# Performance work log

Hardware: AMD Instinct MI355X
Metric: run time of the kernel (lower is better)

Reference implementation:

```python
import jax, jax.numpy as jnp
import numpy as np

MASS = 2.0
B, DIN, H, DOUT = 32768, 4, 128, 5


def setup_inputs():
    key = jax.random.key(0)
    ks = jax.random.split(key, 5)
    def w(k, shp, fan):
        return jax.random.normal(k, shp, jnp.float32) * (1.0 / np.sqrt(fan))
    return {
        "x": jax.random.normal(ks[0], (B, DIN), jnp.float32),
        "W0": w(ks[1], (DIN, H), DIN), "b0": jnp.zeros((H,), jnp.float32),
        "W1": w(ks[2], (H, H), H), "b1": jnp.zeros((H,), jnp.float32),
        "W2": w(ks[3], (H, H), H), "b2": jnp.zeros((H,), jnp.float32),
        "W3": w(ks[4], (H, DOUT), H), "b3": jnp.zeros((DOUT,), jnp.float32),
    }


def _mlp_outs(xs, params):
    # xs: [4] = (t, x, y, z)
    h = xs
    for W, b in params[:-1]:
        h = jnp.tanh(h @ W + b)
    W, b = params[-1]
    o = h @ W + b  # [5]
    return o[:1], o[1:4], o[4:5]  # n [1], v [3], Fi [1]


def _per_sample(xs, params, m):
    outs = lambda z: _mlp_outs(z, params)

    def firsts(z):
        n, v, Fi = outs(z)
        ro = m * n
        return n, n * v, Fi, ro, ro * v  # n, j, Fi, ro, rov

    # all first-order jacobians in one jacfwd pass (4 tangents)
    n_jac, j_jac, Fi_jac, ro_jac, rov_jac = jax.jacfwd(firsts)(xs)

    def pair(z):
        o = outs(z)
        return o[0], o[2]  # n, Fi

    n_hess, Fi_hess = jax.jacfwd(jax.jacfwd(pair))(xs)  # [1,4,4] each

    n, v, Fi = outs(xs)
    n_t = n_jac[..., 0]                                  # [1]
    n_grd = n_jac[..., 1:4]                              # [1,3]
    j = n * v                                            # [3]
    j_div = jnp.sum(j_jac[..., 1:4], axis=-1)            # [3]
    Fi_grd = Fi_jac[..., 1:4]                            # [1,3]
    Fi_lap = jnp.sum(Fi_hess[..., 1:4], axis=-1)         # [1,4]
    # faithful to source: v_jac = batch_jacobian(n, input)  (verbatim bug)
    v_jac = n_jac                                        # [1,4]
    v_t = v_jac[..., 0]                                  # [1]
    v_adv = jnp.sum(v[None, :] * v_jac[..., 1:4], axis=-2)  # [3]
    v_div_jac = jnp.sum(n_hess[:, 1:4, :], axis=1)       # [1,4]
    v_div_grd = v_div_jac[..., 1:4]                      # [1,3]
    v_lap = jnp.trace(n_hess[..., 1:4], axis1=-2, axis2=-1)  # [1]
    ro = m * n                                           # [1]
    ro_t = ro_jac[..., 0]                                # [1]
    ro_grd = ro_jac[..., 1:4]                            # [1,3]
    rov_div = jnp.sum(rov_jac[..., 1:4], axis=-1)        # [3]
    return (n, n_t, n_grd, j, j_div, Fi, Fi_grd, Fi_lap,
            v, v_t, v_adv, v_lap, v_div_grd, ro, ro_t, ro_grd, rov_div)


def reference(x, W0, b0, W1, b1, W2, b2, W3, b3):
    params = [(W0, b0), (W1, b1), (W2, b2), (W3, b3)]
    return jax.vmap(lambda xs: _per_sample(xs, params, MASS))(x)
```

## Files before the change

kernel.cpp:

```cpp
#include <hip/hip_runtime.h>
#include <hip/hip_bf16.h>


namespace {

constexpr int HID = 128;

using bf16x8 = __attribute__((ext_vector_type(8))) short;
using f32x4  = __attribute__((ext_vector_type(4))) float;
typedef unsigned       __attribute__((may_alias)) u32a;
typedef unsigned short __attribute__((may_alias)) u16a;

#define LDS_FENCE() asm volatile("" ::: "memory")

struct OSpec {
    int base, mul, off;
    int a0, a1, a2, m;
    int b0, b1, b2, m2;
    float s1, s2;
};

__constant__ OSpec g_ospec[38] = {
    {0,1,0,   0,80,80,81, 80,80,80,81, 1.f,0.f},
    {1,1,0,   5,80,80,81, 80,80,80,81, 1.f,0.f},
    {2,3,0,  10,80,80,81, 80,80,80,81, 1.f,0.f},
    {2,3,1,  15,80,80,81, 80,80,80,81, 1.f,0.f},
    {2,3,2,  20,80,80,81, 80,80,80,81, 1.f,0.f},
    {5,3,0,   1,80,80, 0, 80,80,80,81, 1.f,0.f},
    {5,3,1,   2,80,80, 0, 80,80,80,81, 1.f,0.f},
    {5,3,2,   3,80,80, 0, 80,80,80,81, 1.f,0.f},
    {8,3,0,  10,15,20, 1, 11,16,21, 0, 1.f,1.f},
    {8,3,1,  10,15,20, 2, 12,17,22, 0, 1.f,1.f},
    {8,3,2,  10,15,20, 3, 13,18,23, 0, 1.f,1.f},
    {11,1,0,  4,80,80,81, 80,80,80,81, 1.f,0.f},
    {12,3,0, 14,80,80,81, 80,80,80,81, 1.f,0.f},
    {12,3,1, 19,80,80,81, 80,80,80,81, 1.f,0.f},
    {12,3,2, 24,80,80,81, 80,80,80,81, 1.f,0.f},
    {15,4,0, 34,39,44,81, 80,80,80,81, 1.f,0.f},
    {15,4,1, 49,54,59,81, 80,80,80,81, 1.f,0.f},
    {15,4,2, 54,64,69,81, 80,80,80,81, 1.f,0.f},
    {15,4,3, 59,69,74,81, 80,80,80,81, 1.f,0.f},
    {19,3,0,  1,80,80,81, 80,80,80,81, 1.f,0.f},
    {19,3,1,  2,80,80,81, 80,80,80,81, 1.f,0.f},
    {19,3,2,  3,80,80,81, 80,80,80,81, 1.f,0.f},
    {22,1,0,  5,80,80,81, 80,80,80,81, 1.f,0.f},
    {23,3,0,  1,80,80,10, 80,80,80,81, 1.f,0.f},
    {23,3,1,  2,80,80,15, 80,80,80,81, 1.f,0.f},
    {23,3,2,  3,80,80,20, 80,80,80,81, 1.f,0.f},
    {26,1,0, 30,50,65,81, 80,80,80,81, 1.f,0.f},
    {27,3,0, 45,50,55,81, 80,80,80,81, 1.f,0.f},
    {27,3,1, 50,60,65,81, 80,80,80,81, 1.f,0.f},
    {27,3,2, 55,65,70,81, 80,80,80,81, 1.f,0.f},
    {30,1,0,  0,80,80,81, 80,80,80,81, 2.f,0.f},
    {31,1,0,  5,80,80,81, 80,80,80,81, 2.f,0.f},
    {32,3,0, 10,80,80,81, 80,80,80,81, 2.f,0.f},
    {32,3,1, 15,80,80,81, 80,80,80,81, 2.f,0.f},
    {32,3,2, 20,80,80,81, 80,80,80,81, 2.f,0.f},
    {35,3,0, 10,15,20, 1, 11,16,21, 0, 2.f,2.f},
    {35,3,1, 10,15,20, 2, 12,17,22, 0, 2.f,2.f},
    {35,3,2, 10,15,20, 3, 13,18,23, 0, 2.f,2.f},
};

__device__ __forceinline__ unsigned short f2bf(float f) {
    union { float f; unsigned u; } v; v.f = f;
    unsigned r = v.u + 0x7FFFu + ((v.u >> 16) & 1u);
    return (unsigned short)(r >> 16);
}
__device__ __forceinline__ unsigned pk_bf16(float lo, float hi) {
    __bf16 l = (__bf16)lo;
    __bf16 h = (__bf16)hi;
    unsigned short ul, uh;
    __builtin_memcpy(&ul, &l, 2);
    __builtin_memcpy(&uh, &h, 2);
    return (unsigned)ul | ((unsigned)uh << 16);
}
__device__ __forceinline__ float tanh_fast(float z) {
    float e = __builtin_amdgcn_exp2f(z * 2.8853900817779268f);
    return 1.0f - 2.0f * __builtin_amdgcn_rcpf(e + 1.0f);
}
__device__ __forceinline__ int swz(int row, int byte_in_row) {
    return (row * 256 + byte_in_row) ^ ((row & 7) << 4);
}

__global__ void pack_w_kernel(const float* __restrict__ W1,
                              const float* __restrict__ W2,
                              const float* __restrict__ W3,
                              unsigned short* __restrict__ wsB) {
    int t = blockIdx.x * 256 + threadIdx.x;
    if (t < 32768) {
        int reg  = t & 7;
        int lane = (t >> 3) & 63;
        int nt   = (t >> 9) & 7;
        int kt   = (t >> 12) & 3;
        int layer = (t >> 14) & 1;
        int k = kt * 32 + (lane >> 4) * 8 + reg;
        int n = nt * 16 + (lane & 15);
        const float* W = layer ? W2 : W1;
        wsB[t] = f2bf(W[k * HID + n]);
    } else if (t < 34816) {
        int tt = t - 32768;
        int reg  = tt & 7;
        int lane = (tt >> 3) & 63;
        int kt   = (tt >> 9) & 3;
        int k = kt * 32 + (lane >> 4) * 8 + reg;
        int n = lane & 15;
        wsB[t] = (n < 5) ? f2bf(W3[k * 5 + n]) : (unsigned short)0;
    }
}

__global__ __launch_bounds__(256, 4) void mlp_pde_kernel(
    const float* __restrict__ x,
    const float* __restrict__ W0, const float* __restrict__ b0,
    const float* __restrict__ b1, const float* __restrict__ b2,
    const float* __restrict__ b3,
    const unsigned short* __restrict__ wsB,
    float* __restrict__ out, int nb)
{
    constexpr int PD[10] = {0,0,0,0,1,1,1,2,2,3};
    constexpr int PE[10] = {0,1,2,3,1,2,3,2,3,3};

    __shared__ float lds[4][2048];
    const int wave = threadIdx.x >> 6;
    const int lane = threadIdx.x & 63;
    float* wbase = lds[wave];
    char* abufA = (char*)wbase;
    char* abufB = (char*)wbase + 4096;
    float* combA = wbase;
    float* combB = wbase + 82;
    int bA = blockIdx.x * 8 + wave * 2;
    int bB = bA + 1;
    if (bA >= nb) bA = nb - 1;
    if (bB >= nb) bB = nb - 1;

    {
        const int j0 = lane * 2;
        float w0d[4][2];
        #pragma unroll
        for (int d = 0; d < 4; ++d) {
            float2 w = *reinterpret_cast<const float2*>(W0 + d * HID + j0);
            w0d[d][0] = w.x; w0d[d][1] = w.y;
        }
        const float2 bb0 = *reinterpret_cast<const float2*>(b0 + j0);
        const float4 xvA = *reinterpret_cast<const float4*>(x + 4 * bA);
        const float4 xvB = *reinterpret_cast<const float4*>(x + 4 * bB);
        #pragma unroll
        for (int s = 0; s < 2; ++s) {
            const float4 xv = s ? xvB : xvA;
            char* abuf = s ? abufB : abufA;
            float val[15][2];
            #pragma unroll
            for (int jj = 0; jj < 2; ++jj) {
                float z = ((jj == 0) ? bb0.x : bb0.y)
                        + xv.x * w0d[0][jj] + xv.y * w0d[1][jj]
                        + xv.z * w0d[2][jj] + xv.w * w0d[3][jj];
                float h = tanh_fast(z);
                float sd = 1.f - h * h;
                val[0][jj] = h;
                #pragma unroll
                for (int d = 0; d < 4; ++d) val[1 + d][jj] = sd * w0d[d][jj];
                #pragma unroll
                for (int p = 0; p < 10; ++p)
                    val[5 + p][jj] = -2.f * h * sd * w0d[PD[p]][jj] * w0d[PE[p]][jj];
            }
            #pragma unroll
            for (int v = 0; v < 15; ++v)
                *reinterpret_cast<u32a*>(abuf + swz(v, j0 * 2)) = pk_bf16(val[v][0], val[v][1]);
            *reinterpret_cast<u32a*>(abuf + swz(15, j0 * 2)) = 0u;
        }
    }
    LDS_FENCE();

    const int jloc = lane & 15;
    const int rgrp = lane >> 4;

    auto recomb = [&](const f32x4& acc, char* abuf, float bnt, int nt) {
        float z0 = __shfl(acc[0], jloc, 64);
        float u0 = __shfl(acc[1], jloc, 64);
        float u1 = __shfl(acc[2], jloc, 64);
        float u2 = __shfl(acc[3], jloc, 64);
        float u3 = __shfl(acc[0], jloc + 16, 64);
        float h = tanh_fast(z0 + bnt);
        float s = 1.f - h * h;
        float c = -2.f * h * s;
        float nv[4];
        if (rgrp == 0) {
            nv[0] = h;           nv[1] = s * u0;
            nv[2] = s * u1;      nv[3] = s * u2;
        } else if (rgrp == 1) {
            nv[0] = s * u3;
            nv[1] = fmaf(c * u0, u0, s * acc[1]);
            nv[2] = fmaf(c * u0, u1, s * acc[2]);
            nv[3] = fmaf(c * u0, u2, s * acc[3]);
        } else if (rgrp == 2) {
            nv[0] = fmaf(c * u0, u3, s * acc[0]);
            nv[1] = fmaf(c * u1, u1, s * acc[1]);
            nv[2] = fmaf(c * u1, u2, s * acc[2]);
            nv[3] = fmaf(c * u1, u3, s * acc[3]);
        } else {
            nv[0] = fmaf(c * u2, u2, s * acc[0]);
            nv[1] = fmaf(c * u2, u3, s * acc[1]);
            nv[2] = fmaf(c * u3, u3, s * acc[2]);
            nv[3] = 0.f;
        }
        unsigned pk01 = pk_bf16(nv[0], nv[1]);
        unsigned pk23 = pk_bf16(nv[2], nv[3]);
        const int bcol = (nt * 16 + jloc) * 2;
        *reinterpret_cast<u16a*>(abuf + swz(rgrp * 4 + 0, bcol)) = (unsigned short)pk01;
        *reinterpret_cast<u16a*>(abuf + swz(rgrp * 4 + 1, bcol)) = (unsigned short)(pk01 >> 16);
        *reinterpret_cast<u16a*>(abuf + swz(rgrp * 4 + 2, bcol)) = (unsigned short)pk23;
        *reinterpret_cast<u16a*>(abuf + swz(rgrp * 4 + 3, bcol)) = (unsigned short)(pk23 >> 16);
    };

    #pragma unroll 1
    for (int layer = 0; layer < 2; ++layer) {
        bf16x8 a0[4], a1[4];
        #pragma unroll
        for (int kt = 0; kt < 4; ++kt) {
            a0[kt] = *reinterpret_cast<const bf16x8*>(abufA + swz(jloc, kt * 64 + rgrp * 16));
            a1[kt] = *reinterpret_cast<const bf16x8*>(abufB + swz(jloc, kt * 64 + rgrp * 16));
        }
        LDS_FENCE();
        const float* bias = layer ? b2 : b1;
        float bv[8];
        #pragma unroll
        for (int nt = 0; nt < 8; ++nt) bv[nt] = bias[nt * 16 + jloc];

        #pragma unroll
        for (int nt = 0; nt < 8; ++nt) {
            f32x4 acc0 = {0.f, 0.f, 0.f, 0.f};
            f32x4 acc1 = {0.f, 0.f, 0.f, 0.f};
            #pragma unroll
            for (int kt = 0; kt < 4; ++kt) {
                bf16x8 bfrag = *reinterpret_cast<const bf16x8*>(
                    wsB + ((size_t)((layer * 4 + kt) * 8 + nt) * 512 + lane * 8));
                acc0 = __builtin_amdgcn_mfma_f32_16x16x32_bf16(a0[kt], bfrag, acc0, 0, 0, 0);
                acc1 = __builtin_amdgcn_mfma_f32_16x16x32_bf16(a1[kt], bfrag, acc1, 0, 0, 0);
            }
            recomb(acc0, abufA, bv[nt], nt);
            recomb(acc1, abufB, bv[nt], nt);
        }
        LDS_FENCE();
    }

    bf16x8 t0[4], t1[4];
    #pragma unroll
    for (int kt = 0; kt < 4; ++kt) {
        t0[kt] = *reinterpret_cast<const bf16x8*>(abufA + swz(jloc, kt * 64 + rgrp * 16));
        t1[kt] = *reinterpret_cast<const bf16x8*>(abufB + swz(jloc, kt * 64 + rgrp * 16));
    }
    LDS_FENCE();

    f32x4 f0 = {0.f, 0.f, 0.f, 0.f};
    f32x4 f1 = {0.f, 0.f, 0.f, 0.f};
    #pragma unroll
    for (int kt = 0; kt < 4; ++kt) {
        bf16x8 w3f = *reinterpret_cast<const bf16x8*>(
            wsB + 32768 + (size_t)(kt * 64 + lane) * 8);
        f0 = __builtin_amdgcn_mfma_f32_16x16x32_bf16(t0[kt], w3f, f0, 0, 0, 0);
        f1 = __builtin_amdgcn_mfma_f32_16x16x32_bf16(t1[kt], w3f, f1, 0, 0, 0);
    }

    if (jloc < 5) {
        #pragma unroll
        for (int q = 0; q < 4; ++q) {
            int row = rgrp * 4 + q;
            float tA = f0[q];
            float tB = f1[q];
            if (row == 0) { float bb = b3[jloc]; tA += bb; tB += bb; }
            combA[row * 5 + jloc] = tA;
            combB[row * 5 + jloc] = tB;
        }
    }
    if (lane == 63) { combA[80] = 0.f; combA[81] = 1.f; combB[80] = 0.f; combB[81] = 1.f; }
    LDS_FENCE();

    if (lane < 38) {
        OSpec sp = g_ospec[lane];
        float a1v = (combA[sp.a0] + combA[sp.a1] + combA[sp.a2]) * combA[sp.m] * sp.s1;
        float a2v = (combA[sp.b0] + combA[sp.b1] + combA[sp.b2]) * combA[sp.m2] * sp.s2;
        out[sp.base * nb + bA * sp.mul + sp.off] = a1v + a2v;
        float c1v = (combB[sp.a0] + combB[sp.a1] + combB[sp.a2]) * combB[sp.m] * sp.s1;
        float c2v = (combB[sp.b0] + combB[sp.b1] + combB[sp.b2]) * combB[sp.m2] * sp.s2;
        out[sp.base * nb + bB * sp.mul + sp.off] = c1v + c2v;
    }
}

}

extern "C" void kernel_launch(void* const* d_in, const int* in_sizes, int n_in,
                              void* d_out, int out_size, void* d_ws, size_t ws_size,
                              hipStream_t stream) {
    const float* x  = (const float*)d_in[0];
    const float* W0 = (const float*)d_in[1];
    const float* b0 = (const float*)d_in[2];
    const float* W1 = (const float*)d_in[3];
    const float* b1 = (const float*)d_in[4];
    const float* W2 = (const float*)d_in[5];
    const float* b2 = (const float*)d_in[6];
    const float* W3 = (const float*)d_in[7];
    const float* b3 = (const float*)d_in[8];
    float* out = (float*)d_out;
    unsigned short* wsB = (unsigned short*)d_ws;

    const int nb = in_sizes[0] / 4;
    pack_w_kernel<<<136, 256, 0, stream>>>(W1, W2, W3, wsB);
    const int blocks = (nb + 7) / 8;
    mlp_pde_kernel<<<blocks, 256, 0, stream>>>(x, W0, b0, b1, b2, b3, wsB, out, nb);
}
```

Measured before the change: 82.83 us.

## Switch hidden-layer MFMAs to 32x32x16 tiles covering both samples per wave

```diff
diff --git a/kernel.cpp b/kernel.cpp
--- a/kernel.cpp
+++ b/kernel.cpp
@@ -7,7 +7,7 @@
 constexpr int HID = 128;
 
 using bf16x8 = __attribute__((ext_vector_type(8))) short;
-using f32x4  = __attribute__((ext_vector_type(4))) float;
+using f32x16 = __attribute__((ext_vector_type(16))) float;
 typedef unsigned       __attribute__((may_alias)) u32a;
 typedef unsigned short __attribute__((may_alias)) u16a;
 
@@ -23,42 +23,42 @@
 __constant__ OSpec g_ospec[38] = {
     {0,1,0,   0,80,80,81, 80,80,80,81, 1.f,0.f},
     {1,1,0,   5,80,80,81, 80,80,80,81, 1.f,0.f},
-    {2,3,0,  10,80,80,81, 80,80,80,81, 1.f,0.f},
-    {2,3,1,  15,80,80,81, 80,80,80,81, 1.f,0.f},
-    {2,3,2,  20,80,80,81, 80,80,80,81, 1.f,0.f},
+    {2,3,0,  25,80,80,81, 80,80,80,81, 1.f,0.f},
+    {2,3,1,  10,80,80,81, 80,80,80,81, 1.f,0.f},
+    {2,3,2,  30,80,80,81, 80,80,80,81, 1.f,0.f},
     {5,3,0,   1,80,80, 0, 80,80,80,81, 1.f,0.f},
     {5,3,1,   2,80,80, 0, 80,80,80,81, 1.f,0.f},
     {5,3,2,   3,80,80, 0, 80,80,80,81, 1.f,0.f},
-    {8,3,0,  10,15,20, 1, 11,16,21, 0, 1.f,1.f},
-    {8,3,1,  10,15,20, 2, 12,17,22, 0, 1.f,1.f},
-    {8,3,2,  10,15,20, 3, 13,18,23, 0, 1.f,1.f},
+    {8,3,0,  25,10,30, 1, 26,11,31, 0, 1.f,1.f},
+    {8,3,1,  25,10,30, 2, 27,12,32, 0, 1.f,1.f},
+    {8,3,2,  25,10,30, 3, 28,13,33, 0, 1.f,1.f},
     {11,1,0,  4,80,80,81, 80,80,80,81, 1.f,0.f},
-    {12,3,0, 14,80,80,81, 80,80,80,81, 1.f,0.f},
-    {12,3,1, 19,80,80,81, 80,80,80,81, 1.f,0.f},
-    {12,3,2, 24,80,80,81, 80,80,80,81, 1.f,0.f},
-    {15,4,0, 34,39,44,81, 80,80,80,81, 1.f,0.f},
-    {15,4,1, 49,54,59,81, 80,80,80,81, 1.f,0.f},
-    {15,4,2, 54,64,69,81, 80,80,80,81, 1.f,0.f},
-    {15,4,3, 59,69,74,81, 80,80,80,81, 1.f,0.f},
+    {12,3,0, 29,80,80,81, 80,80,80,81, 1.f,0.f},
+    {12,3,1, 14,80,80,81, 80,80,80,81, 1.f,0.f},
+    {12,3,2, 34,80,80,81, 80,80,80,81, 1.f,0.f},
+    {15,4,0, 39,44,64,81, 80,80,80,81, 1.f,0.f},
+    {15,4,1, 49,69,54,81, 80,80,80,81, 1.f,0.f},
+    {15,4,2, 69,74,59,81, 80,80,80,81, 1.f,0.f},
+    {15,4,3, 54,59,79,81, 80,80,80,81, 1.f,0.f},
     {19,3,0,  1,80,80,81, 80,80,80,81, 1.f,0.f},
     {19,3,1,  2,80,80,81, 80,80,80,81, 1.f,0.f},
     {19,3,2,  3,80,80,81, 80,80,80,81, 1.f,0.f},
     {22,1,0,  5,80,80,81, 80,80,80,81, 1.f,0.f},
-    {23,3,0,  1,80,80,10, 80,80,80,81, 1.f,0.f},
-    {23,3,1,  2,80,80,15, 80,80,80,81, 1.f,0.f},
-    {23,3,2,  3,80,80,20, 80,80,80,81, 1.f,0.f},
-    {26,1,0, 30,50,65,81, 80,80,80,81, 1.f,0.f},
-    {27,3,0, 45,50,55,81, 80,80,80,81, 1.f,0.f},
-    {27,3,1, 50,60,65,81, 80,80,80,81, 1.f,0.f},
-    {27,3,2, 55,65,70,81, 80,80,80,81, 1.f,0.f},
+    {23,3,0,  1,80,80,25, 80,80,80,81, 1.f,0.f},
+    {23,3,1,  2,80,80,10, 80,80,80,81, 1.f,0.f},
+    {23,3,2,  3,80,80,30, 80,80,80,81, 1.f,0.f},
+    {26,1,0, 35,65,55,81, 80,80,80,81, 1.f,0.f},
+    {27,3,0, 45,65,50,81, 80,80,80,81, 1.f,0.f},
+    {27,3,1, 65,70,55,81, 80,80,80,81, 1.f,0.f},
+    {27,3,2, 50,55,75,81, 80,80,80,81, 1.f,0.f},
     {30,1,0,  0,80,80,81, 80,80,80,81, 2.f,0.f},
     {31,1,0,  5,80,80,81, 80,80,80,81, 2.f,0.f},
-    {32,3,0, 10,80,80,81, 80,80,80,81, 2.f,0.f},
-    {32,3,1, 15,80,80,81, 80,80,80,81, 2.f,0.f},
-    {32,3,2, 20,80,80,81, 80,80,80,81, 2.f,0.f},
-    {35,3,0, 10,15,20, 1, 11,16,21, 0, 2.f,2.f},
-    {35,3,1, 10,15,20, 2, 12,17,22, 0, 2.f,2.f},
-    {35,3,2, 10,15,20, 3, 13,18,23, 0, 2.f,2.f},
+    {32,3,0, 25,80,80,81, 80,80,80,81, 2.f,0.f},
+    {32,3,1, 10,80,80,81, 80,80,80,81, 2.f,0.f},
+    {32,3,2, 30,80,80,81, 80,80,80,81, 2.f,0.f},
+    {35,3,0, 25,10,30, 1, 26,11,31, 0, 2.f,2.f},
+    {35,3,1, 25,10,30, 2, 27,12,32, 0, 2.f,2.f},
+    {35,3,2, 25,10,30, 3, 28,13,33, 0, 2.f,2.f},
 };
 
 __device__ __forceinline__ unsigned short f2bf(float f) {
@@ -74,6 +74,10 @@
     __builtin_memcpy(&uh, &h, 2);
     return (unsigned)ul | ((unsigned)uh << 16);
 }
+__device__ __forceinline__ unsigned short bf1(float x) {
+    __bf16 b = (__bf16)x;
+    unsigned short u; __builtin_memcpy(&u, &b, 2); return u;
+}
 __device__ __forceinline__ float tanh_fast(float z) {
     float e = __builtin_amdgcn_exp2f(z * 2.8853900817779268f);
     return 1.0f - 2.0f * __builtin_amdgcn_rcpf(e + 1.0f);
@@ -88,22 +92,22 @@
                               unsigned short* __restrict__ wsB) {
     int t = blockIdx.x * 256 + threadIdx.x;
     if (t < 32768) {
-        int reg  = t & 7;
-        int lane = (t >> 3) & 63;
-        int nt   = (t >> 9) & 7;
-        int kt   = (t >> 12) & 3;
+        int reg   = t & 7;
+        int lane  = (t >> 3) & 63;
+        int tile  = (t >> 9) & 3;
+        int kt    = (t >> 11) & 7;
         int layer = (t >> 14) & 1;
-        int k = kt * 32 + (lane >> 4) * 8 + reg;
-        int n = nt * 16 + (lane & 15);
+        int k = kt * 16 + ((lane >> 5) & 1) * 8 + reg;
+        int n = tile * 32 + (lane & 31);
         const float* W = layer ? W2 : W1;
         wsB[t] = f2bf(W[k * HID + n]);
-    } else if (t < 34816) {
+    } else if (t < 36864) {
         int tt = t - 32768;
         int reg  = tt & 7;
         int lane = (tt >> 3) & 63;
-        int kt   = (tt >> 9) & 3;
-        int k = kt * 32 + (lane >> 4) * 8 + reg;
-        int n = lane & 15;
+        int kt   = (tt >> 9) & 7;
+        int k = kt * 16 + ((lane >> 5) & 1) * 8 + reg;
+        int n = lane & 31;
         wsB[t] = (n < 5) ? f2bf(W3[k * 5 + n]) : (unsigned short)0;
     }
 }
@@ -118,6 +122,8 @@
 {
     constexpr int PD[10] = {0,0,0,0,1,1,1,2,2,3};
     constexpr int PE[10] = {0,1,2,3,1,2,3,2,3,3};
+    constexpr int ROWMAP[15] = {0,1,5,2,6,3,7,8,12,9,13,10,14,11,15};
+    constexpr int RB[8] = {0,1,2,3,8,9,10,11};
 
     __shared__ float lds[4][2048];
     const int wave = threadIdx.x >> 6;
@@ -164,111 +170,112 @@
             }
             #pragma unroll
             for (int v = 0; v < 15; ++v)
-                *reinterpret_cast<u32a*>(abuf + swz(v, j0 * 2)) = pk_bf16(val[v][0], val[v][1]);
-            *reinterpret_cast<u32a*>(abuf + swz(15, j0 * 2)) = 0u;
+                *reinterpret_cast<u32a*>(abuf + swz(ROWMAP[v], j0 * 2)) =
+                    pk_bf16(val[v][0], val[v][1]);
+            *reinterpret_cast<u32a*>(abuf + swz(4, j0 * 2)) = 0u;
         }
     }
     LDS_FENCE();
 
-    const int jloc = lane & 15;
-    const int rgrp = lane >> 4;
-
-    auto recomb = [&](const f32x4& acc, char* abuf, float bnt, int nt) {
-        float z0 = __shfl(acc[0], jloc, 64);
-        float u0 = __shfl(acc[1], jloc, 64);
-        float u1 = __shfl(acc[2], jloc, 64);
-        float u2 = __shfl(acc[3], jloc, 64);
-        float u3 = __shfl(acc[0], jloc + 16, 64);
-        float h = tanh_fast(z0 + bnt);
-        float s = 1.f - h * h;
-        float c = -2.f * h * s;
-        float nv[4];
-        if (rgrp == 0) {
-            nv[0] = h;           nv[1] = s * u0;
-            nv[2] = s * u1;      nv[3] = s * u2;
-        } else if (rgrp == 1) {
-            nv[0] = s * u3;
-            nv[1] = fmaf(c * u0, u0, s * acc[1]);
-            nv[2] = fmaf(c * u0, u1, s * acc[2]);
-            nv[3] = fmaf(c * u0, u2, s * acc[3]);
-        } else if (rgrp == 2) {
-            nv[0] = fmaf(c * u0, u3, s * acc[0]);
-            nv[1] = fmaf(c * u1, u1, s * acc[1]);
-            nv[2] = fmaf(c * u1, u2, s * acc[2]);
-            nv[3] = fmaf(c * u1, u3, s * acc[3]);
-        } else {
-            nv[0] = fmaf(c * u2, u2, s * acc[0]);
-            nv[1] = fmaf(c * u2, u3, s * acc[1]);
-            nv[2] = fmaf(c * u3, u3, s * acc[2]);
-            nv[3] = 0.f;
-        }
-        unsigned pk01 = pk_bf16(nv[0], nv[1]);
-        unsigned pk23 = pk_bf16(nv[2], nv[3]);
-        const int bcol = (nt * 16 + jloc) * 2;
-        *reinterpret_cast<u16a*>(abuf + swz(rgrp * 4 + 0, bcol)) = (unsigned short)pk01;
-        *reinterpret_cast<u16a*>(abuf + swz(rgrp * 4 + 1, bcol)) = (unsigned short)(pk01 >> 16);
-        *reinterpret_cast<u16a*>(abuf + swz(rgrp * 4 + 2, bcol)) = (unsigned short)pk23;
-        *reinterpret_cast<u16a*>(abuf + swz(rgrp * 4 + 3, bcol)) = (unsigned short)(pk23 >> 16);
-    };
+    const int col  = lane & 31;
+    const int hi   = lane >> 5;
+    const int arow = lane & 15;
+    char* abufM = (char*)wbase + ((lane >> 4) & 1) * 4096;
 
     #pragma unroll 1
     for (int layer = 0; layer < 2; ++layer) {
-        bf16x8 a0[4], a1[4];
-        #pragma unroll
-        for (int kt = 0; kt < 4; ++kt) {
-            a0[kt] = *reinterpret_cast<const bf16x8*>(abufA + swz(jloc, kt * 64 + rgrp * 16));
-            a1[kt] = *reinterpret_cast<const bf16x8*>(abufB + swz(jloc, kt * 64 + rgrp * 16));
+        bf16x8 af[8];
+        #pragma unroll
+        for (int kt = 0; kt < 8; ++kt)
+            af[kt] = *reinterpret_cast<const bf16x8*>(
+                abufM + swz(arow, kt * 32 + hi * 16));
+        LDS_FENCE();
+        const float* bias = layer ? b2 : b1;
+        float bv[4];
+        #pragma unroll
+        for (int t4 = 0; t4 < 4; ++t4) bv[t4] = bias[t4 * 32 + col];
+
+        #pragma unroll
+        for (int t4 = 0; t4 < 4; ++t4) {
+            f32x16 acc = {0.f,0.f,0.f,0.f,0.f,0.f,0.f,0.f,
+                          0.f,0.f,0.f,0.f,0.f,0.f,0.f,0.f};
+            #pragma unroll
+            for (int kt = 0; kt < 8; ++kt) {
+                bf16x8 bfrag = *reinterpret_cast<const bf16x8*>(
+                    wsB + ((size_t)(((layer * 8 + kt) * 4) + t4) * 512 + lane * 8));
+                acc = __builtin_amdgcn_mfma_f32_32x32x16_bf16(af[kt], bfrag, acc, 0, 0, 0);
+            }
+            float zA  = __shfl(acc[0],  col,      64);
+            float uA0 = __shfl(acc[1],  col,      64);
+            float uA1 = __shfl(acc[1],  col + 32, 64);
+            float uA2 = __shfl(acc[2],  col,      64);
+            float uA3 = __shfl(acc[2],  col + 32, 64);
+            float zB  = __shfl(acc[8],  col,      64);
+            float uB0 = __shfl(acc[9],  col,      64);
+            float uB1 = __shfl(acc[9],  col + 32, 64);
+            float uB2 = __shfl(acc[10], col,      64);
+            float uB3 = __shfl(acc[10], col + 32, 64);
+            float hA = tanh_fast(zA + bv[t4]);
+            float sA = 1.f - hA * hA;  float cA = -2.f * hA * sA;
+            float hB = tanh_fast(zB + bv[t4]);
+            float sB = 1.f - hB * hB;  float cB = -2.f * hB * sB;
+            const bool H = (hi != 0);
+
+            float nvA[8], nvB[8];
+            nvA[0] = H ? 0.f : hA;
+            nvA[1] = sA * (H ? uA1 : uA0);
+            nvA[2] = sA * (H ? uA3 : uA2);
+            nvA[3] = fmaf(cA * uA0, H ? uA1 : uA0, sA * acc[3]);
+            nvA[4] = fmaf(cA * uA0, H ? uA3 : uA2, sA * acc[4]);
+            nvA[5] = fmaf(cA * uA1, H ? uA2 : uA1, sA * acc[5]);
+            nvA[6] = fmaf(cA * (H ? uA2 : uA1), H ? uA2 : uA3, sA * acc[6]);
+            nvA[7] = fmaf(cA * (H ? uA3 : uA2), uA3, sA * acc[7]);
+            nvB[0] = H ? 0.f : hB;
+            nvB[1] = sB * (H ? uB1 : uB0);
+            nvB[2] = sB * (H ? uB3 : uB2);
+            nvB[3] = fmaf(cB * uB0, H ? uB1 : uB0, sB * acc[11]);
+            nvB[4] = fmaf(cB * uB0, H ? uB3 : uB2, sB * acc[12]);
+            nvB[5] = fmaf(cB * uB1, H ? uB2 : uB1, sB * acc[13]);
+            nvB[6] = fmaf(cB * (H ? uB2 : uB1), H ? uB2 : uB3, sB * acc[14]);
+            nvB[7] = fmaf(cB * (H ? uB3 : uB2), uB3, sB * acc[15]);
+
+            const int cb = (t4 * 32 + col) * 2;
+            #pragma unroll
+            for (int q = 0; q < 8; ++q) {
+                int rowq = RB[q] + 4 * hi;
+                *reinterpret_cast<u16a*>(abufA + swz(rowq, cb)) = bf1(nvA[q]);
+                *reinterpret_cast<u16a*>(abufB + swz(rowq, cb)) = bf1(nvB[q]);
+            }
         }
         LDS_FENCE();
-        const float* bias = layer ? b2 : b1;
-        float bv[8];
-        #pragma unroll
-        for (int nt = 0; nt < 8; ++nt) bv[nt] = bias[nt * 16 + jloc];
-
-        #pragma unroll
-        for (int nt = 0; nt < 8; ++nt) {
-            f32x4 acc0 = {0.f, 0.f, 0.f, 0.f};
-            f32x4 acc1 = {0.f, 0.f, 0.f, 0.f};
-            #pragma unroll
-            for (int kt = 0; kt < 4; ++kt) {
-                bf16x8 bfrag = *reinterpret_cast<const bf16x8*>(
-                    wsB + ((size_t)((layer * 4 + kt) * 8 + nt) * 512 + lane * 8));
-                acc0 = __builtin_amdgcn_mfma_f32_16x16x32_bf16(a0[kt], bfrag, acc0, 0, 0, 0);
-                acc1 = __builtin_amdgcn_mfma_f32_16x16x32_bf16(a1[kt], bfrag, acc1, 0, 0, 0);
-            }
-            recomb(acc0, abufA, bv[nt], nt);
-            recomb(acc1, abufB, bv[nt], nt);
-        }
-        LDS_FENCE();
-    }
-
-    bf16x8 t0[4], t1[4];
+    }
+
+    bf16x8 tf[8];
     #pragma unroll
-    for (int kt = 0; kt < 4; ++kt) {
-        t0[kt] = *reinterpret_cast<const bf16x8*>(abufA + swz(jloc, kt * 64 + rgrp * 16));
-        t1[kt] = *reinterpret_cast<const bf16x8*>(abufB + swz(jloc, kt * 64 + rgrp * 16));
-    }
+    for (int kt = 0; kt < 8; ++kt)
+        tf[kt] = *reinterpret_cast<const bf16x8*>(
+            abufM + swz(arow, kt * 32 + hi * 16));
     LDS_FENCE();
 
-    f32x4 f0 = {0.f, 0.f, 0.f, 0.f};
-    f32x4 f1 = {0.f, 0.f, 0.f, 0.f};
+    f32x16 fa = {0.f,0.f,0.f,0.f,0.f,0.f,0.f,0.f,
+                 0.f,0.f,0.f,0.f,0.f,0.f,0.f,0.f};
     #pragma unroll
-    for (int kt = 0; kt < 4; ++kt) {
+    for (int kt = 0; kt < 8; ++kt) {
         bf16x8 w3f = *reinterpret_cast<const bf16x8*>(
-            wsB + 32768 + (size_t)(kt * 64 + lane) * 8);
-        f0 = __builtin_amdgcn_mfma_f32_16x16x32_bf16(t0[kt], w3f, f0, 0, 0, 0);
-        f1 = __builtin_amdgcn_mfma_f32_16x16x32_bf16(t1[kt], w3f, f1, 0, 0, 0);
-    }
-
-    if (jloc < 5) {
-        #pragma unroll
-        for (int q = 0; q < 4; ++q) {
-            int row = rgrp * 4 + q;
-            float tA = f0[q];
-            float tB = f1[q];
-            if (row == 0) { float bb = b3[jloc]; tA += bb; tB += bb; }
-            combA[row * 5 + jloc] = tA;
-            combB[row * 5 + jloc] = tB;
+            wsB + 32768 + (size_t)(kt * 512 + lane * 8));
+        fa = __builtin_amdgcn_mfma_f32_32x32x16_bf16(tf[kt], w3f, fa, 0, 0, 0);
+    }
+
+    if (col < 5) {
+        float badd = (hi != 0) ? 0.f : b3[col];
+        #pragma unroll
+        for (int q = 0; q < 8; ++q) {
+            int rowq = RB[q] + 4 * hi;
+            float tA = fa[q];
+            float tB = fa[q + 8];
+            if (q == 0) { tA += badd; tB += badd; }
+            combA[rowq * 5 + col] = tA;
+            combB[rowq * 5 + col] = tB;
         }
     }
     if (lane == 63) { combA[80] = 0.f; combA[81] = 1.f; combB[80] = 0.f; combB[81] = 1.f; }
@@ -303,7 +310,7 @@
     unsigned short* wsB = (unsigned short*)d_ws;
 
     const int nb = in_sizes[0] / 4;
-    pack_w_kernel<<<136, 256, 0, stream>>>(W1, W2, W3, wsB);
+    pack_w_kernel<<<144, 256, 0, stream>>>(W1, W2, W3, wsB);
     const int blocks = (nb + 7) / 8;
     mlp_pde_kernel<<<blocks, 256, 0, stream>>>(x, W0, b0, b1, b2, b3, wsB, out, nb);
 }
```

Result: no change. 81.79 us (-1.3%).
